# Kernel optimization log

Hardware: AMD Instinct MI355X
Metric: run time of the kernel (lower is better)

## Reference

```python
import jax, jax.numpy as jnp
import numpy as np

B, T, DP, DQ, DO = 128, 2048, 256, 256, 256


def setup_inputs() -> dict:
    key = jax.random.key(0)
    ks = jax.random.split(key, 10)
    return {
        "input_p": jax.random.normal(ks[0], (B, DP), dtype=jnp.float32),
        "mask_p": jnp.ones((B,), dtype=jnp.float32),
        "input_q": jax.random.normal(ks[1], (B, T, DQ), dtype=jnp.float32),
        "mask_q": jax.random.randint(ks[2], (B, T), 0, 2, dtype=jnp.int32),
        "h_tm1": jax.random.normal(ks[3], (B, DO), dtype=jnp.float32),
        # layer-0 parameters (depth == 0)
        "W_p_r": jax.random.normal(ks[4], (DO, DP + DO), dtype=jnp.float32) * 0.04,
        "b_p_r": jnp.zeros((DO,), dtype=jnp.float32),
        "W_q": jax.random.normal(ks[5], (DO, DQ), dtype=jnp.float32) * 0.05,
        "b_q": jnp.zeros((DO,), dtype=jnp.float32),
        "w": jax.random.normal(ks[6], (DO,), dtype=jnp.float32) * 0.05,
        "match_b": jnp.ones((1,), dtype=jnp.float32),
        "depth": 0,
    }


def masked_softmax(x, m, axis=-1):
    x = jnp.clip(x, -15.0, 15.0)
    x = x * m
    e_x = jnp.exp(x - jnp.max(x, axis=axis, keepdims=True))
    e_x = e_x * m
    return e_x / (jnp.sum(e_x, axis=axis, keepdims=True) + 1e-6)


def reference(input_p, mask_p, input_q, mask_q, h_tm1, W_p_r, b_p_r, W_q, b_q, w, match_b, depth):
    mq = mask_q.astype(jnp.float32)
    # G_p_r: [B, 1, DO]
    G_p_r = (jnp.concatenate([input_p, h_tm1], axis=-1) @ W_p_r.T + b_p_r)[:, None, :]
    # G_q: [B, T, DO]
    G_q = input_q @ W_q.T + b_q
    G = jnp.tanh(G_p_r + G_q)
    alpha = jnp.einsum("btd,d->bt", G, w) + match_b  # [B, T]
    alpha = masked_softmax(alpha, mq, axis=-1)
    z = jnp.einsum("bt,btd->bd", alpha, input_q)  # bmm context
    return jnp.concatenate([input_p, z], axis=1)  # [B, DP+DQ]
```

## Files before the change

### kernel.cpp

```cpp
#include <hip/hip_runtime.h>
#include <hip/hip_bf16.h>

typedef short short8 __attribute__((ext_vector_type(8)));
typedef float floatx4 __attribute__((ext_vector_type(4)));

constexpr int Bn = 128, Tn = 2048, DPn = 256, DQn = 256, DOn = 256;
constexpr int NCH = Tn / 64;

__device__ inline unsigned pk2(float x, float y) {
    __hip_bfloat162 h = __float22bfloat162_rn(make_float2(x, y));
    return *(unsigned*)&h;
}
__device__ inline float fast_tanh(float x) {
    float e = __expf(2.0f * x);
    return 1.0f - 2.0f / (e + 1.0f);
}

__global__ __launch_bounds__(256) void prep_kernel(const float* __restrict__ wq,
                                                   unsigned short* __restrict__ wqbf,
                                                   const float* __restrict__ input_p,
                                                   const float* __restrict__ h_tm1,
                                                   const float* __restrict__ Wpr,
                                                   const float* __restrict__ bpr,
                                                   const float* __restrict__ bq,
                                                   float* __restrict__ base) {
    __shared__ float v[512];
    int tid = threadIdx.x;
    if (blockIdx.x < 64) {
        int idx = blockIdx.x * 256 + tid;
        float4 x = ((const float4*)wq)[idx];
        ((uint2*)wqbf)[idx] = make_uint2(pk2(x.x, x.y), pk2(x.z, x.w));
        return;
    }
    int b = blockIdx.x - 64;
    v[tid]       = input_p[b * DPn + tid];
    v[256 + tid] = h_tm1[b * DOn + tid];
    __syncthreads();
    const float4* row = (const float4*)(Wpr + (size_t)tid * 512);
    const float4* vv  = (const float4*)v;
    float acc = 0.f;
#pragma unroll 8
    for (int i = 0; i < 128; i++) {
        float4 r = row[i], x = vv[i];
        acc = fmaf(r.x, x.x, acc);
        acc = fmaf(r.y, x.y, acc);
        acc = fmaf(r.z, x.z, acc);
        acc = fmaf(r.w, x.w, acc);
    }
    base[b * DOn + tid] = acc + bpr[tid] + bq[tid];
}

__global__ __launch_bounds__(256, 2) void fused_kernel(const float* __restrict__ q,
                                                       const unsigned short* __restrict__ wqbf,
                                                       const float* __restrict__ base,
                                                       const float* __restrict__ wvec,
                                                       const float* __restrict__ matchb,
                                                       const int* __restrict__ maskq,
                                                       float* __restrict__ zpart,
                                                       float* __restrict__ spart,
                                                       float* __restrict__ mpart) {
    __shared__ __align__(16) float tile[64 * 256];
    __shared__ __align__(16) float zp[4][256];
    __shared__ float partl[4][64];
    __shared__ float earr[64];

    int b = blockIdx.y, c = blockIdx.x;
    int t0 = c * 64;
    int tid = threadIdx.x;
    int w = tid >> 6, lane = tid & 63, l15 = lane & 15, quad = lane >> 4;
    char* tb = (char*)tile;

    {
        const float* qsrc = q + ((size_t)b * Tn + t0) * DQn;
#pragma unroll
        for (int i = 0; i < 16; i++) {
            int r = w * 16 + i;
            float4 x = *(const float4*)(qsrc + (size_t)r * DQn + lane * 4);
            *(float4*)(tb + r * 1024 + ((lane * 16) ^ ((r & 7) << 4))) = x;
        }
    }

    short8 bfr[4][8];
    const unsigned short* bbase = wqbf + (size_t)(w * 64 + l15) * 256 + quad * 8;
#pragma unroll
    for (int nt = 0; nt < 4; nt++)
#pragma unroll
        for (int ks = 0; ks < 8; ks++)
            bfr[nt][ks] = *(const short8*)(bbase + nt * 16 * 256 + ks * 32);
    float bn[4], wn[4];
#pragma unroll
    for (int nt = 0; nt < 4; nt++) {
        int n = w * 64 + nt * 16 + l15;
        bn[nt] = base[b * DOn + n];
        wn[nt] = wvec[n];
    }
    __syncthreads();

#pragma unroll
    for (int mt = 0; mt < 4; mt++) {
        int r = mt * 16 + l15;
        const char* ab = tb + r * 1024;
        int swz = (r & 7) << 4;
        short8 af[8];
#pragma unroll
        for (int ks = 0; ks < 8; ks++) {
            int cb = quad * 32 + ks * 128;
            float4 f0 = *(const float4*)(ab + (cb ^ swz));
            float4 f1 = *(const float4*)(ab + ((cb + 16) ^ swz));
            union { unsigned u[4]; short8 s; } cv;
            cv.u[0] = pk2(f0.x, f0.y);
            cv.u[1] = pk2(f0.z, f0.w);
            cv.u[2] = pk2(f1.x, f1.y);
            cv.u[3] = pk2(f1.z, f1.w);
            af[ks] = cv.s;
        }
        float prow[4] = {0.f, 0.f, 0.f, 0.f};
#pragma unroll
        for (int nt = 0; nt < 4; nt++) {
            floatx4 acc = {0.f, 0.f, 0.f, 0.f};
#pragma unroll
            for (int ks = 0; ks < 8; ks++)
                acc = __builtin_amdgcn_mfma_f32_16x16x32_bf16(af[ks], bfr[nt][ks], acc, 0, 0, 0);
#pragma unroll
            for (int rr = 0; rr < 4; rr++) {
                float g = fast_tanh(acc[rr] + bn[nt]);
                prow[rr] = fmaf(g, wn[nt], prow[rr]);
            }
        }
#pragma unroll
        for (int off = 1; off < 16; off <<= 1)
#pragma unroll
            for (int rr = 0; rr < 4; rr++) prow[rr] += __shfl_xor(prow[rr], off);
        if (l15 == 0) {
#pragma unroll
            for (int rr = 0; rr < 4; rr++) partl[w][mt * 16 + quad * 4 + rr] = prow[rr];
        }
    }
    __syncthreads();

    if (tid < 64) {
        int t = tid;
        float lg = partl[0][t] + partl[1][t] + partl[2][t] + partl[3][t] + matchb[0];
        float m = (float)maskq[(size_t)b * Tn + t0 + t];
        float x = fminf(fmaxf(lg, -15.f), 15.f) * m;
        float e = __expf(x - 15.f) * m;
        earr[t] = e;
        float xm = x, es = e;
#pragma unroll
        for (int off = 1; off < 64; off <<= 1) {
            xm = fmaxf(xm, __shfl_xor(xm, off));
            es += __shfl_xor(es, off);
        }
        if (t == 0) {
            mpart[b * NCH + c] = xm;
            spart[b * NCH + c] = es;
        }
    }
    __syncthreads();

    {
        float a0 = 0.f, a1 = 0.f, a2 = 0.f, a3 = 0.f;
#pragma unroll
        for (int i = 0; i < 16; i++) {
            int r = w * 16 + i;
            float e = earr[r];
            float4 x = *(const float4*)(tb + r * 1024 + ((lane * 16) ^ ((r & 7) << 4)));
            a0 = fmaf(e, x.x, a0);
            a1 = fmaf(e, x.y, a1);
            a2 = fmaf(e, x.z, a2);
            a3 = fmaf(e, x.w, a3);
        }
        *(float4*)&zp[w][lane * 4] = make_float4(a0, a1, a2, a3);
    }
    __syncthreads();
    {
        float zs = zp[0][tid] + zp[1][tid] + zp[2][tid] + zp[3][tid];
        zpart[((size_t)b * NCH + c) * DQn + tid] = zs;
    }
}

__global__ __launch_bounds__(256) void final_kernel(const float* __restrict__ input_p,
                                                    const float* __restrict__ zpart,
                                                    const float* __restrict__ spart,
                                                    const float* __restrict__ mpart,
                                                    float* __restrict__ out) {
    int b = blockIdx.x, tid = threadIdx.x;
    float S = 0.f, mx = -1e30f;
#pragma unroll 8
    for (int c = 0; c < NCH; c++) {
        S += spart[b * NCH + c];
        mx = fmaxf(mx, mpart[b * NCH + c]);
    }
    float denom = S + 1e-6f * __expf(mx - 15.f);
    float inv = 1.0f / denom;
    float zs = 0.f;
#pragma unroll 8
    for (int c = 0; c < NCH; c++) zs += zpart[((size_t)b * NCH + c) * DQn + tid];
    out[(size_t)b * 512 + tid] = input_p[(size_t)b * DPn + tid];
    out[(size_t)b * 512 + 256 + tid] = zs * inv;
}

extern "C" void kernel_launch(void* const* d_in, const int* in_sizes, int n_in,
                              void* d_out, int out_size, void* d_ws, size_t ws_size,
                              hipStream_t stream) {
    const float* input_p = (const float*)d_in[0];
    const float* input_q = (const float*)d_in[2];
    const int*   mask_q  = (const int*)d_in[3];
    const float* h_tm1   = (const float*)d_in[4];
    const float* W_p_r   = (const float*)d_in[5];
    const float* b_p_r   = (const float*)d_in[6];
    const float* W_q     = (const float*)d_in[7];
    const float* b_q     = (const float*)d_in[8];
    const float* w       = (const float*)d_in[9];
    const float* match_b = (const float*)d_in[10];
    float* out = (float*)d_out;

    char* ws = (char*)d_ws;
    unsigned short* wqbf = (unsigned short*)ws;
    float* base  = (float*)(ws + 131072);
    float* zpart = (float*)(ws + 262144);
    float* spart = (float*)(ws + 262144 + 4194304);
    float* mpart = (float*)(ws + 262144 + 4194304 + 16384);

    prep_kernel<<<192, 256, 0, stream>>>(W_q, wqbf, input_p, h_tm1, W_p_r, b_p_r, b_q, base);
    fused_kernel<<<dim3(NCH, Bn), 256, 0, stream>>>(input_q, wqbf, base, w, match_b,
                                                    mask_q, zpart, spart, mpart);
    final_kernel<<<Bn, 256, 0, stream>>>(input_p, zpart, spart, mpart, out);
}
```

Baseline: 427.9 us.

## Loop each block over multiple T chunks to reuse Wq fragments

Each fused block now processes 8 consecutive 64-row chunks of the sequence instead of one. It keeps the bf16 Wq register fragments, bias and w vector loaded across chunks and accumulates the context, sum and max locally before writing one partial per group. This cuts redundant weight loads and partial writes and shrinks the final reduction. The prep kernel also splits each batch's G_p_r dot products across two blocks with a shared-memory partial sum. The trade-off is fewer blocks in flight (512), so there is less latency hiding between the global loads and the compute, which now run serially within each block.

```diff
diff --git a/kernel.cpp b/kernel.cpp
--- a/kernel.cpp
+++ b/kernel.cpp
@@ -5,7 +5,8 @@
 typedef float floatx4 __attribute__((ext_vector_type(4)));
 
 constexpr int Bn = 128, Tn = 2048, DPn = 256, DQn = 256, DOn = 256;
-constexpr int NCH = Tn / 64;
+constexpr int GB = 4;
+constexpr int CPB = 8;
 
 __device__ inline unsigned pk2(float x, float y) {
     __hip_bfloat162 h = __float22bfloat162_rn(make_float2(x, y));
@@ -25,6 +26,7 @@
                                                    const float* __restrict__ bq,
                                                    float* __restrict__ base) {
     __shared__ float v[512];
+    __shared__ float ps[128];
     int tid = threadIdx.x;
     if (blockIdx.x < 64) {
         int idx = blockIdx.x * 256 + tid;
@@ -32,22 +34,27 @@
         ((uint2*)wqbf)[idx] = make_uint2(pk2(x.x, x.y), pk2(x.z, x.w));
         return;
     }
-    int b = blockIdx.x - 64;
+    int bi = blockIdx.x - 64;
+    int b = bi >> 1, half = bi & 1;
     v[tid]       = input_p[b * DPn + tid];
     v[256 + tid] = h_tm1[b * DOn + tid];
     __syncthreads();
-    const float4* row = (const float4*)(Wpr + (size_t)tid * 512);
-    const float4* vv  = (const float4*)v;
+    int dl = tid & 127, seg = tid >> 7;
+    int d = half * 128 + dl;
+    const float4* row = (const float4*)(Wpr + (size_t)d * 512 + seg * 256);
+    const float4* vv  = (const float4*)(v + seg * 256);
     float acc = 0.f;
 #pragma unroll 8
-    for (int i = 0; i < 128; i++) {
+    for (int i = 0; i < 64; i++) {
         float4 r = row[i], x = vv[i];
         acc = fmaf(r.x, x.x, acc);
         acc = fmaf(r.y, x.y, acc);
         acc = fmaf(r.z, x.z, acc);
         acc = fmaf(r.w, x.w, acc);
     }
-    base[b * DOn + tid] = acc + bpr[tid] + bq[tid];
+    if (seg) ps[dl] = acc;
+    __syncthreads();
+    if (!seg) base[b * DOn + d] = acc + ps[dl] + bpr[d] + bq[d];
 }
 
 __global__ __launch_bounds__(256, 2) void fused_kernel(const float* __restrict__ q,
@@ -64,21 +71,10 @@
     __shared__ float partl[4][64];
     __shared__ float earr[64];
 
-    int b = blockIdx.y, c = blockIdx.x;
-    int t0 = c * 64;
+    int b = blockIdx.y, g = blockIdx.x;
     int tid = threadIdx.x;
     int w = tid >> 6, lane = tid & 63, l15 = lane & 15, quad = lane >> 4;
     char* tb = (char*)tile;
-
-    {
-        const float* qsrc = q + ((size_t)b * Tn + t0) * DQn;
-#pragma unroll
-        for (int i = 0; i < 16; i++) {
-            int r = w * 16 + i;
-            float4 x = *(const float4*)(qsrc + (size_t)r * DQn + lane * 4);
-            *(float4*)(tb + r * 1024 + ((lane * 16) ^ ((r & 7) << 4))) = x;
-        }
-    }
 
     short8 bfr[4][8];
     const unsigned short* bbase = wqbf + (size_t)(w * 64 + l15) * 256 + quad * 8;
@@ -94,88 +90,107 @@
         bn[nt] = base[b * DOn + n];
         wn[nt] = wvec[n];
     }
-    __syncthreads();
-
-#pragma unroll
-    for (int mt = 0; mt < 4; mt++) {
-        int r = mt * 16 + l15;
-        const char* ab = tb + r * 1024;
-        int swz = (r & 7) << 4;
-        short8 af[8];
-#pragma unroll
-        for (int ks = 0; ks < 8; ks++) {
-            int cb = quad * 32 + ks * 128;
-            float4 f0 = *(const float4*)(ab + (cb ^ swz));
-            float4 f1 = *(const float4*)(ab + ((cb + 16) ^ swz));
-            union { unsigned u[4]; short8 s; } cv;
-            cv.u[0] = pk2(f0.x, f0.y);
-            cv.u[1] = pk2(f0.z, f0.w);
-            cv.u[2] = pk2(f1.x, f1.y);
-            cv.u[3] = pk2(f1.z, f1.w);
-            af[ks] = cv.s;
-        }
-        float prow[4] = {0.f, 0.f, 0.f, 0.f};
-#pragma unroll
-        for (int nt = 0; nt < 4; nt++) {
-            floatx4 acc = {0.f, 0.f, 0.f, 0.f};
-#pragma unroll
-            for (int ks = 0; ks < 8; ks++)
-                acc = __builtin_amdgcn_mfma_f32_16x16x32_bf16(af[ks], bfr[nt][ks], acc, 0, 0, 0);
-#pragma unroll
-            for (int rr = 0; rr < 4; rr++) {
-                float g = fast_tanh(acc[rr] + bn[nt]);
-                prow[rr] = fmaf(g, wn[nt], prow[rr]);
-            }
-        }
-#pragma unroll
-        for (int off = 1; off < 16; off <<= 1)
-#pragma unroll
-            for (int rr = 0; rr < 4; rr++) prow[rr] += __shfl_xor(prow[rr], off);
-        if (l15 == 0) {
-#pragma unroll
-            for (int rr = 0; rr < 4; rr++) partl[w][mt * 16 + quad * 4 + rr] = prow[rr];
-        }
-    }
-    __syncthreads();
-
-    if (tid < 64) {
-        int t = tid;
-        float lg = partl[0][t] + partl[1][t] + partl[2][t] + partl[3][t] + matchb[0];
-        float m = (float)maskq[(size_t)b * Tn + t0 + t];
-        float x = fminf(fmaxf(lg, -15.f), 15.f) * m;
-        float e = __expf(x - 15.f) * m;
-        earr[t] = e;
-        float xm = x, es = e;
-#pragma unroll
-        for (int off = 1; off < 64; off <<= 1) {
-            xm = fmaxf(xm, __shfl_xor(xm, off));
-            es += __shfl_xor(es, off);
-        }
-        if (t == 0) {
-            mpart[b * NCH + c] = xm;
-            spart[b * NCH + c] = es;
-        }
-    }
-    __syncthreads();
-
-    {
-        float a0 = 0.f, a1 = 0.f, a2 = 0.f, a3 = 0.f;
-#pragma unroll
-        for (int i = 0; i < 16; i++) {
-            int r = w * 16 + i;
-            float e = earr[r];
-            float4 x = *(const float4*)(tb + r * 1024 + ((lane * 16) ^ ((r & 7) << 4)));
-            a0 = fmaf(e, x.x, a0);
-            a1 = fmaf(e, x.y, a1);
-            a2 = fmaf(e, x.z, a2);
-            a3 = fmaf(e, x.w, a3);
-        }
-        *(float4*)&zp[w][lane * 4] = make_float4(a0, a1, a2, a3);
-    }
-    __syncthreads();
-    {
-        float zs = zp[0][tid] + zp[1][tid] + zp[2][tid] + zp[3][tid];
-        zpart[((size_t)b * NCH + c) * DQn + tid] = zs;
+    float mb = matchb[0];
+
+    float zacc = 0.f;
+    float sacc = 0.f, macc = -1e30f;
+
+    for (int cc = 0; cc < CPB; cc++) {
+        int t0 = (g * CPB + cc) * 64;
+
+        {
+            const float* qsrc = q + ((size_t)b * Tn + t0) * DQn;
+#pragma unroll
+            for (int i = 0; i < 16; i++) {
+                int r = w * 16 + i;
+                float4 x = *(const float4*)(qsrc + (size_t)r * DQn + lane * 4);
+                *(float4*)(tb + r * 1024 + ((lane * 16) ^ ((r & 7) << 4))) = x;
+            }
+        }
+        __syncthreads();
+
+#pragma unroll
+        for (int mt = 0; mt < 4; mt++) {
+            int r = mt * 16 + l15;
+            const char* ab = tb + r * 1024;
+            int swz = (r & 7) << 4;
+            short8 af[8];
+#pragma unroll
+            for (int ks = 0; ks < 8; ks++) {
+                int cb = quad * 32 + ks * 128;
+                float4 f0 = *(const float4*)(ab + (cb ^ swz));
+                float4 f1 = *(const float4*)(ab + ((cb + 16) ^ swz));
+                union { unsigned u[4]; short8 s; } cv;
+                cv.u[0] = pk2(f0.x, f0.y);
+                cv.u[1] = pk2(f0.z, f0.w);
+                cv.u[2] = pk2(f1.x, f1.y);
+                cv.u[3] = pk2(f1.z, f1.w);
+                af[ks] = cv.s;
+            }
+            float prow[4] = {0.f, 0.f, 0.f, 0.f};
+#pragma unroll
+            for (int nt = 0; nt < 4; nt++) {
+                floatx4 acc = {0.f, 0.f, 0.f, 0.f};
+#pragma unroll
+                for (int ks = 0; ks < 8; ks++)
+                    acc = __builtin_amdgcn_mfma_f32_16x16x32_bf16(af[ks], bfr[nt][ks], acc, 0, 0, 0);
+#pragma unroll
+                for (int rr = 0; rr < 4; rr++) {
+                    float gg = fast_tanh(acc[rr] + bn[nt]);
+                    prow[rr] = fmaf(gg, wn[nt], prow[rr]);
+                }
+            }
+#pragma unroll
+            for (int off = 1; off < 16; off <<= 1)
+#pragma unroll
+                for (int rr = 0; rr < 4; rr++) prow[rr] += __shfl_xor(prow[rr], off);
+            if (l15 == 0) {
+#pragma unroll
+                for (int rr = 0; rr < 4; rr++) partl[w][mt * 16 + quad * 4 + rr] = prow[rr];
+            }
+        }
+        __syncthreads();
+
+        if (tid < 64) {
+            int t = tid;
+            float lg = partl[0][t] + partl[1][t] + partl[2][t] + partl[3][t] + mb;
+            float m = (float)maskq[(size_t)b * Tn + t0 + t];
+            float x = fminf(fmaxf(lg, -15.f), 15.f) * m;
+            float e = __expf(x - 15.f) * m;
+            earr[t] = e;
+            float xm = x, es = e;
+#pragma unroll
+            for (int off = 1; off < 64; off <<= 1) {
+                xm = fmaxf(xm, __shfl_xor(xm, off));
+                es += __shfl_xor(es, off);
+            }
+            macc = fmaxf(macc, xm);
+            sacc += es;
+        }
+        __syncthreads();
+
+        {
+            float a0 = 0.f, a1 = 0.f, a2 = 0.f, a3 = 0.f;
+#pragma unroll
+            for (int i = 0; i < 16; i++) {
+                int r = w * 16 + i;
+                float e = earr[r];
+                float4 x = *(const float4*)(tb + r * 1024 + ((lane * 16) ^ ((r & 7) << 4)));
+                a0 = fmaf(e, x.x, a0);
+                a1 = fmaf(e, x.y, a1);
+                a2 = fmaf(e, x.z, a2);
+                a3 = fmaf(e, x.w, a3);
+            }
+            *(float4*)&zp[w][lane * 4] = make_float4(a0, a1, a2, a3);
+        }
+        __syncthreads();
+        zacc += zp[0][tid] + zp[1][tid] + zp[2][tid] + zp[3][tid];
+    }
+
+    zpart[((size_t)b * GB + g) * DQn + tid] = zacc;
+    if (tid == 0) {
+        mpart[b * GB + g] = macc;
+        spart[b * GB + g] = sacc;
     }
 }
 
@@ -186,16 +201,16 @@
                                                     float* __restrict__ out) {
     int b = blockIdx.x, tid = threadIdx.x;
     float S = 0.f, mx = -1e30f;
-#pragma unroll 8
-    for (int c = 0; c < NCH; c++) {
-        S += spart[b * NCH + c];
-        mx = fmaxf(mx, mpart[b * NCH + c]);
+#pragma unroll
+    for (int c = 0; c < GB; c++) {
+        S += spart[b * GB + c];
+        mx = fmaxf(mx, mpart[b * GB + c]);
     }
     float denom = S + 1e-6f * __expf(mx - 15.f);
     float inv = 1.0f / denom;
     float zs = 0.f;
-#pragma unroll 8
-    for (int c = 0; c < NCH; c++) zs += zpart[((size_t)b * NCH + c) * DQn + tid];
+#pragma unroll
+    for (int c = 0; c < GB; c++) zs += zpart[((size_t)b * GB + c) * DQn + tid];
     out[(size_t)b * 512 + tid] = input_p[(size_t)b * DPn + tid];
     out[(size_t)b * 512 + 256 + tid] = zs * inv;
 }
@@ -219,11 +234,11 @@
     unsigned short* wqbf = (unsigned short*)ws;
     float* base  = (float*)(ws + 131072);
     float* zpart = (float*)(ws + 262144);
-    float* spart = (float*)(ws + 262144 + 4194304);
-    float* mpart = (float*)(ws + 262144 + 4194304 + 16384);
-
-    prep_kernel<<<192, 256, 0, stream>>>(W_q, wqbf, input_p, h_tm1, W_p_r, b_p_r, b_q, base);
-    fused_kernel<<<dim3(NCH, Bn), 256, 0, stream>>>(input_q, wqbf, base, w, match_b,
-                                                    mask_q, zpart, spart, mpart);
+    float* spart = (float*)(ws + 262144 + 524288);
+    float* mpart = (float*)(ws + 262144 + 524288 + 16384);
+
+    prep_kernel<<<320, 256, 0, stream>>>(W_q, wqbf, input_p, h_tm1, W_p_r, b_p_r, b_q, base);
+    fused_kernel<<<dim3(GB, Bn), 256, 0, stream>>>(input_q, wqbf, base, w, match_b,
+                                                   mask_q, zpart, spart, mpart);
     final_kernel<<<Bn, 256, 0, stream>>>(input_p, zpart, spart, mpart, out);
 }
```

Measured after the change: 451.3 us. 1.05x slower.

## Halve attention chunk size, stream W_q fragments, raise occupancy, split prep GEMV

Applied to the files above, without the earlier changes.

Shrinks the per-block time chunk from 64 to 32 rows, cutting LDS use and registers so four blocks per CU can be resident. W_q bf16 fragments are now loaded per n-tile instead of all held in registers up front. Softmax weights move through wave shuffles instead of shared memory, which removes one barrier. The prep GEMV is split across two blocks per batch row, each handling half the outputs with a two-way K split. The costs are twice as many partial-sum blocks, more zpart traffic and more final-reduction work, and the W_q fragments are now reloaded by twice as many blocks.

```diff
diff --git a/kernel.cpp b/kernel.cpp
--- a/kernel.cpp
+++ b/kernel.cpp
@@ -5,7 +5,8 @@
 typedef float floatx4 __attribute__((ext_vector_type(4)));
 
 constexpr int Bn = 128, Tn = 2048, DPn = 256, DQn = 256, DOn = 256;
-constexpr int NCH = Tn / 64;
+constexpr int RCH = 32;
+constexpr int NCH = Tn / RCH;
 
 __device__ inline unsigned pk2(float x, float y) {
     __hip_bfloat162 h = __float22bfloat162_rn(make_float2(x, y));
@@ -25,6 +26,7 @@
                                                    const float* __restrict__ bq,
                                                    float* __restrict__ base) {
     __shared__ float v[512];
+    __shared__ float ps[128];
     int tid = threadIdx.x;
     if (blockIdx.x < 64) {
         int idx = blockIdx.x * 256 + tid;
@@ -32,25 +34,30 @@
         ((uint2*)wqbf)[idx] = make_uint2(pk2(x.x, x.y), pk2(x.z, x.w));
         return;
     }
-    int b = blockIdx.x - 64;
+    int bi = blockIdx.x - 64;
+    int b = bi >> 1, half = bi & 1;
     v[tid]       = input_p[b * DPn + tid];
     v[256 + tid] = h_tm1[b * DOn + tid];
     __syncthreads();
-    const float4* row = (const float4*)(Wpr + (size_t)tid * 512);
-    const float4* vv  = (const float4*)v;
+    int dl = tid & 127, seg = tid >> 7;
+    int d = half * 128 + dl;
+    const float4* row = (const float4*)(Wpr + (size_t)d * 512 + seg * 256);
+    const float4* vv  = (const float4*)(v + seg * 256);
     float acc = 0.f;
 #pragma unroll 8
-    for (int i = 0; i < 128; i++) {
+    for (int i = 0; i < 64; i++) {
         float4 r = row[i], x = vv[i];
         acc = fmaf(r.x, x.x, acc);
         acc = fmaf(r.y, x.y, acc);
         acc = fmaf(r.z, x.z, acc);
         acc = fmaf(r.w, x.w, acc);
     }
-    base[b * DOn + tid] = acc + bpr[tid] + bq[tid];
-}
-
-__global__ __launch_bounds__(256, 2) void fused_kernel(const float* __restrict__ q,
+    if (seg) ps[dl] = acc;
+    __syncthreads();
+    if (!seg) base[b * DOn + d] = acc + ps[dl] + bpr[d] + bq[d];
+}
+
+__global__ __launch_bounds__(256, 4) void fused_kernel(const float* __restrict__ q,
                                                        const unsigned short* __restrict__ wqbf,
                                                        const float* __restrict__ base,
                                                        const float* __restrict__ wvec,
@@ -59,112 +66,115 @@
                                                        float* __restrict__ zpart,
                                                        float* __restrict__ spart,
                                                        float* __restrict__ mpart) {
-    __shared__ __align__(16) float tile[64 * 256];
+    __shared__ __align__(16) float tile[RCH * 256];
     __shared__ __align__(16) float zp[4][256];
-    __shared__ float partl[4][64];
-    __shared__ float earr[64];
+    __shared__ __align__(16) float partl[32][4];
 
     int b = blockIdx.y, c = blockIdx.x;
-    int t0 = c * 64;
+    int t0 = c * RCH;
     int tid = threadIdx.x;
     int w = tid >> 6, lane = tid & 63, l15 = lane & 15, quad = lane >> 4;
     char* tb = (char*)tile;
+    float mb = matchb[0];
 
     {
         const float* qsrc = q + ((size_t)b * Tn + t0) * DQn;
 #pragma unroll
-        for (int i = 0; i < 16; i++) {
-            int r = w * 16 + i;
+        for (int i = 0; i < 8; i++) {
+            int r = w * 8 + i;
             float4 x = *(const float4*)(qsrc + (size_t)r * DQn + lane * 4);
             *(float4*)(tb + r * 1024 + ((lane * 16) ^ ((r & 7) << 4))) = x;
         }
     }
-
-    short8 bfr[4][8];
-    const unsigned short* bbase = wqbf + (size_t)(w * 64 + l15) * 256 + quad * 8;
-#pragma unroll
-    for (int nt = 0; nt < 4; nt++)
-#pragma unroll
-        for (int ks = 0; ks < 8; ks++)
-            bfr[nt][ks] = *(const short8*)(bbase + nt * 16 * 256 + ks * 32);
-    float bn[4], wn[4];
-#pragma unroll
-    for (int nt = 0; nt < 4; nt++) {
-        int n = w * 64 + nt * 16 + l15;
-        bn[nt] = base[b * DOn + n];
-        wn[nt] = wvec[n];
-    }
-    __syncthreads();
-
-#pragma unroll
-    for (int mt = 0; mt < 4; mt++) {
-        int r = mt * 16 + l15;
-        const char* ab = tb + r * 1024;
-        int swz = (r & 7) << 4;
-        short8 af[8];
-#pragma unroll
-        for (int ks = 0; ks < 8; ks++) {
-            int cb = quad * 32 + ks * 128;
-            float4 f0 = *(const float4*)(ab + (cb ^ swz));
-            float4 f1 = *(const float4*)(ab + ((cb + 16) ^ swz));
-            union { unsigned u[4]; short8 s; } cv;
-            cv.u[0] = pk2(f0.x, f0.y);
-            cv.u[1] = pk2(f0.z, f0.w);
-            cv.u[2] = pk2(f1.x, f1.y);
-            cv.u[3] = pk2(f1.z, f1.w);
-            af[ks] = cv.s;
-        }
-        float prow[4] = {0.f, 0.f, 0.f, 0.f};
+    __syncthreads();
+
+    short8 af[2][8];
+    {
+        int swz = (l15 & 7) << 4;
+#pragma unroll
+        for (int mt = 0; mt < 2; mt++) {
+            const char* ab = tb + (mt * 16 + l15) * 1024;
+#pragma unroll
+            for (int ks = 0; ks < 8; ks++) {
+                int cb = quad * 32 + ks * 128;
+                float4 f0 = *(const float4*)(ab + (cb ^ swz));
+                float4 f1 = *(const float4*)(ab + ((cb + 16) ^ swz));
+                union { unsigned u[4]; short8 s; } cv;
+                cv.u[0] = pk2(f0.x, f0.y);
+                cv.u[1] = pk2(f0.z, f0.w);
+                cv.u[2] = pk2(f1.x, f1.y);
+                cv.u[3] = pk2(f1.z, f1.w);
+                af[mt][ks] = cv.s;
+            }
+        }
+    }
+    float prow[2][4] = {{0.f, 0.f, 0.f, 0.f}, {0.f, 0.f, 0.f, 0.f}};
+    {
+        const unsigned short* bbase = wqbf + (size_t)(w * 64 + l15) * 256 + quad * 8;
 #pragma unroll
         for (int nt = 0; nt < 4; nt++) {
-            floatx4 acc = {0.f, 0.f, 0.f, 0.f};
+            short8 bfr[8];
 #pragma unroll
             for (int ks = 0; ks < 8; ks++)
-                acc = __builtin_amdgcn_mfma_f32_16x16x32_bf16(af[ks], bfr[nt][ks], acc, 0, 0, 0);
-#pragma unroll
-            for (int rr = 0; rr < 4; rr++) {
-                float g = fast_tanh(acc[rr] + bn[nt]);
-                prow[rr] = fmaf(g, wn[nt], prow[rr]);
+                bfr[ks] = *(const short8*)(bbase + nt * 16 * 256 + ks * 32);
+            int n = w * 64 + nt * 16 + l15;
+            float bnv = base[b * DOn + n];
+            float wnv = wvec[n];
+#pragma unroll
+            for (int mt = 0; mt < 2; mt++) {
+                floatx4 acc = {0.f, 0.f, 0.f, 0.f};
+#pragma unroll
+                for (int ks = 0; ks < 8; ks++)
+                    acc = __builtin_amdgcn_mfma_f32_16x16x32_bf16(af[mt][ks], bfr[ks], acc, 0, 0, 0);
+#pragma unroll
+                for (int rr = 0; rr < 4; rr++) {
+                    float gg = fast_tanh(acc[rr] + bnv);
+                    prow[mt][rr] = fmaf(gg, wnv, prow[mt][rr]);
+                }
             }
         }
-#pragma unroll
-        for (int off = 1; off < 16; off <<= 1)
-#pragma unroll
-            for (int rr = 0; rr < 4; rr++) prow[rr] += __shfl_xor(prow[rr], off);
-        if (l15 == 0) {
-#pragma unroll
-            for (int rr = 0; rr < 4; rr++) partl[w][mt * 16 + quad * 4 + rr] = prow[rr];
-        }
-    }
-    __syncthreads();
-
-    if (tid < 64) {
-        int t = tid;
-        float lg = partl[0][t] + partl[1][t] + partl[2][t] + partl[3][t] + matchb[0];
+    }
+#pragma unroll
+    for (int off = 1; off < 16; off <<= 1)
+#pragma unroll
+        for (int mt = 0; mt < 2; mt++)
+#pragma unroll
+            for (int rr = 0; rr < 4; rr++) prow[mt][rr] += __shfl_xor(prow[mt][rr], off);
+    if (l15 == 0) {
+#pragma unroll
+        for (int mt = 0; mt < 2; mt++)
+#pragma unroll
+            for (int rr = 0; rr < 4; rr++) partl[mt * 16 + quad * 4 + rr][w] = prow[mt][rr];
+    }
+    __syncthreads();
+
+    float ew;
+    {
+        int t = lane & 31;
+        float4 pl = *(const float4*)&partl[t][0];
+        float lg = pl.x + pl.y + pl.z + pl.w + mb;
         float m = (float)maskq[(size_t)b * Tn + t0 + t];
         float x = fminf(fmaxf(lg, -15.f), 15.f) * m;
-        float e = __expf(x - 15.f) * m;
-        earr[t] = e;
-        float xm = x, es = e;
-#pragma unroll
-        for (int off = 1; off < 64; off <<= 1) {
+        ew = __expf(x - 15.f) * m;
+        float xm = x, es = ew;
+#pragma unroll
+        for (int off = 1; off < 32; off <<= 1) {
             xm = fmaxf(xm, __shfl_xor(xm, off));
             es += __shfl_xor(es, off);
         }
-        if (t == 0) {
+        if (tid == 0) {
             mpart[b * NCH + c] = xm;
             spart[b * NCH + c] = es;
         }
     }
-    __syncthreads();
 
     {
         float a0 = 0.f, a1 = 0.f, a2 = 0.f, a3 = 0.f;
 #pragma unroll
-        for (int i = 0; i < 16; i++) {
-            int r = w * 16 + i;
-            float e = earr[r];
-            float4 x = *(const float4*)(tb + r * 1024 + ((lane * 16) ^ ((r & 7) << 4)));
+        for (int i = 0; i < 8; i++) {
+            int r = w * 8 + i;
+            float e = __shfl(ew, r);
+            float4 x = *(const float4*)(tb + r * 1024 + ((lane * 16) ^ (i << 4)));
             a0 = fmaf(e, x.x, a0);
             a1 = fmaf(e, x.y, a1);
             a2 = fmaf(e, x.z, a2);
@@ -219,10 +229,10 @@
     unsigned short* wqbf = (unsigned short*)ws;
     float* base  = (float*)(ws + 131072);
     float* zpart = (float*)(ws + 262144);
-    float* spart = (float*)(ws + 262144 + 4194304);
-    float* mpart = (float*)(ws + 262144 + 4194304 + 16384);
-
-    prep_kernel<<<192, 256, 0, stream>>>(W_q, wqbf, input_p, h_tm1, W_p_r, b_p_r, b_q, base);
+    float* spart = (float*)(ws + 262144 + 8388608);
+    float* mpart = (float*)(ws + 262144 + 8388608 + 32768);
+
+    prep_kernel<<<320, 256, 0, stream>>>(W_q, wqbf, input_p, h_tm1, W_p_r, b_p_r, b_q, base);
     fused_kernel<<<dim3(NCH, Bn), 256, 0, stream>>>(input_q, wqbf, base, w, match_b,
                                                     mask_q, zpart, spart, mpart);
     final_kernel<<<Bn, 256, 0, stream>>>(input_p, zpart, spart, mpart, out);
```

After: 482.9 us. +12.8%, slower.
